# Kernel tuning notes

Measured on AMD Instinct MI355X. Metric: run time of the kernel, lower is better.

The kernel has to match this reference:

```python
import jax, jax.numpy as jnp
import numpy as np

N_NODES = 200000
N_EDGES = 6400000
N_GRAPHS = 512
VOCAB = 10
EMBED = 8
RLEN = 20
EPS = 1e-5


def setup_inputs() -> dict:
    key = jax.random.key(0)
    ks = jax.random.split(key, 16)
    f = lambda i, shape, s: jax.random.normal(ks[i], shape, jnp.float32) * s
    return {
        "x": jax.random.normal(ks[0], (N_NODES, 3), jnp.float32),
        "W1": f(1, (3, 64), 0.5), "b1": jnp.zeros((64,), jnp.float32),
        "gamma1": jnp.ones((64,), jnp.float32), "beta1": jnp.zeros((64,), jnp.float32),
        "W2": f(2, (64, 64), 0.12), "b2": jnp.zeros((64,), jnp.float32),
        "gamma2": jnp.ones((64,), jnp.float32), "beta2": jnp.zeros((64,), jnp.float32),
        "emb": f(3, (VOCAB, EMBED), 1.0),
        "conv_w": f(4, (16, EMBED, 3), 0.2), "conv_b": jnp.zeros((16,), jnp.float32),
        "fc_w": f(5, (16 * RLEN, 64), 0.06), "fc_b": jnp.zeros((64,), jnp.float32),
        "m1_w": f(6, (192, 128), 0.08), "m1_b": jnp.zeros((128,), jnp.float32),
        "m2_w": f(7, (128, 64), 0.1), "m2_b": jnp.zeros((64,), jnp.float32),
        "m3_w": f(8, (64, 3), 0.17), "m3_b": jnp.zeros((3,), jnp.float32),
        "edge_index": jax.random.randint(ks[9], (2, N_EDGES), 0, N_NODES),
        "batch": jnp.sort(jax.random.randint(ks[10], (N_NODES,), 0, N_GRAPHS)),
        "recipe": jax.random.randint(ks[11], (N_GRAPHS, RLEN), 0, VOCAB),
    }


def _gcn_aggregate(h, src, dst, dinv, n):
    # symmetric-normalized scatter-add: sum_j (d_i d_j)^{-1/2} h_j
    norm = dinv[src] * dinv[dst]
    return jax.ops.segment_sum(h[src] * norm[:, None], dst, num_segments=n)


def _bn(h, gamma, beta):
    mu = h.mean(0)
    var = h.var(0)  # biased variance, as torch BN uses for normalization
    return (h - mu) * jax.lax.rsqrt(var + EPS) * gamma + beta


def reference(x, W1, b1, gamma1, beta1, W2, b2, gamma2, beta2, emb,
              conv_w, conv_b, fc_w, fc_b, m1_w, m1_b, m2_w, m2_b, m3_w, m3_b,
              edge_index, batch, recipe):
    n = x.shape[0]
    loop = jnp.arange(n)
    src = jnp.concatenate([edge_index[0], loop])  # add self loops (GCNConv default)
    dst = jnp.concatenate([edge_index[1], loop])
    deg = jax.ops.segment_sum(jnp.ones_like(src, jnp.float32), dst, num_segments=n)
    dinv = jnp.where(deg > 0, jax.lax.rsqrt(deg), 0.0)

    h = _gcn_aggregate(x @ W1, src, dst, dinv, n) + b1
    h = jax.nn.relu(_bn(h, gamma1, beta1))
    h = _gcn_aggregate(h @ W2, src, dst, dinv, n) + b2
    h = jax.nn.relu(_bn(h, gamma2, beta2))

    counts = jax.ops.segment_sum(jnp.ones((n,), jnp.float32), batch, num_segments=N_GRAPHS)
    h_mean = jax.ops.segment_sum(h, batch, num_segments=N_GRAPHS) / jnp.maximum(counts, 1.0)[:, None]
    h_max = jax.ops.segment_max(h, batch, num_segments=N_GRAPHS)
    h_max = jnp.where(jnp.isfinite(h_max), h_max, 0.0)  # guard empty graphs
    h_graph = jnp.concatenate([h_mean, h_max], axis=1)  # [G, 128]

    r = emb[recipe].transpose(0, 2, 1)  # [G, embed, L]
    rc = jax.lax.conv_general_dilated(r, conv_w, window_strides=(1,), padding=[(1, 1)],
                                      dimension_numbers=("NCH", "OIH", "NCH"))
    rc = jax.nn.relu(rc + conv_b[None, :, None])  # [G, 16, L]
    r_flat = rc.reshape(rc.shape[0], -1)  # channel-major flatten, matches torch
    r_vec = jax.nn.relu(r_flat @ fc_w + fc_b)  # [G, 64]

    c = jnp.concatenate([h_graph, r_vec], axis=1)  # [G, 192]
    c = jax.nn.relu(c @ m1_w + m1_b)
    c = jax.nn.relu(c @ m2_w + m2_b)
    return c @ m3_w + m3_b  # [G, 3]
```

## Files before the change

kernel.cpp:

```cpp
#include <hip/hip_runtime.h>

#define N_NODES 200000
#define N_EDGES 6400000
#define N_GRAPHS 512
#define RLEN 20
#define EMBED 8
#define EPS 1e-5f

#define NPB 1024
#define NBKT ((N_NODES + NPB - 1) / NPB)
#define CHUNK 8192
#define CAP 36864

typedef unsigned short ushort_t;
typedef __attribute__((ext_vector_type(8))) short short8;
typedef __attribute__((ext_vector_type(4))) float f32x4;

__device__ inline ushort_t f32_to_bf16(float f) {
  unsigned u = __float_as_uint(f);
  unsigned r = (u + 0x7fff + ((u >> 16) & 1)) >> 16;
  return (ushort_t)r;
}
__device__ inline float bf16_to_f32(ushort_t us) {
  return __uint_as_float(((unsigned)us) << 16);
}
__device__ inline float bfu_lo(unsigned u) { return __uint_as_float(u << 16); }
__device__ inline float bfu_hi(unsigned u) { return __uint_as_float(u & 0xFFFF0000u); }


__global__ void __launch_bounds__(512) k_bscatter(const int* __restrict__ src,
                                                  const int* __restrict__ dst,
                                                  int* __restrict__ bcursor,
                                                  int* __restrict__ ebuf) {
  __shared__ int hist[8][256];
  __shared__ int gbase[256];
  int t = threadIdx.x;
  int wid = t >> 6;
  for (int i = t; i < 8 * 256; i += 512) ((int*)hist)[i] = 0;
  __syncthreads();

  const int4* src4 = (const int4*)(src + blockIdx.x * CHUNK);
  const int4* dst4 = (const int4*)(dst + blockIdx.x * CHUNK);
  int e0 = blockIdx.x * CHUNK;
  int nrem = N_EDGES - e0;
  int nv = (nrem >= CHUNK ? CHUNK : nrem) >> 2;

  int pk[16], bk[16], rk[16];
  #pragma unroll
  for (int g = 0; g < 4; ++g) {
    int vi = g * 512 + t;
    if (vi < nv) {
      int4 s4 = src4[vi];
      int4 d4 = dst4[vi];
      #pragma unroll
      for (int c = 0; c < 4; ++c) {
        int s = (&s4.x)[c], d = (&d4.x)[c];
        int b = d >> 10;
        pk[g * 4 + c] = s | ((d & (NPB - 1)) << 18);
        bk[g * 4 + c] = b;
        rk[g * 4 + c] = atomicAdd(&hist[wid][b], 1);
      }
    } else {
      #pragma unroll
      for (int c = 0; c < 4; ++c) bk[g * 4 + c] = -1;
    }
  }
  __syncthreads();
  if (t < 256) {
    int s = 0;
    #pragma unroll
    for (int w = 0; w < 8; ++w) { int v = hist[w][t]; hist[w][t] = s; s += v; }
    if (t < NBKT && s > 0) gbase[t] = t * CAP + atomicAdd(&bcursor[t], s);
  }
  __syncthreads();
  #pragma unroll
  for (int k = 0; k < 16; ++k) {
    if (bk[k] >= 0) ebuf[gbase[bk[k]] + hist[wid][bk[k]] + rk[k]] = pk[k];
  }
}

__global__ void __launch_bounds__(1024) k_bfill(const int* __restrict__ bcursor,
                                                const int* __restrict__ ebuf,
                                                const float* __restrict__ x,
                                                int* __restrict__ rowstart,
                                                int* __restrict__ rowlen,
                                                float* __restrict__ dinv,
                                                float4* __restrict__ xs,
                                                int* __restrict__ cols) {
  __shared__ int deg[NPB];
  __shared__ int cur[NPB];
  __shared__ int wsum[16];
  int b = blockIdx.x;
  int t = threadIdx.x;
  int lane = t & 63, wid = t >> 6;
  int estart = b * CAP;
  int cnt = bcursor[b];
  int eend = estart + cnt;
  int nv = cnt >> 2;
  const int4* eb4 = (const int4*)(ebuf + estart);
  deg[t] = 0;
  __syncthreads();
  for (int i = t; i < nv; i += 1024) {
    int4 p4 = eb4[i];
    atomicAdd(&deg[((unsigned)p4.x) >> 18], 1);
    atomicAdd(&deg[((unsigned)p4.y) >> 18], 1);
    atomicAdd(&deg[((unsigned)p4.z) >> 18], 1);
    atomicAdd(&deg[((unsigned)p4.w) >> 18], 1);
  }
  for (int i = estart + (nv << 2) + t; i < eend; i += 1024) {
    int p = ebuf[i];
    atomicAdd(&deg[((unsigned)p) >> 18], 1);
  }
  __syncthreads();
  int v = deg[t];
  int incl = v;
  #pragma unroll
  for (int off = 1; off < 64; off <<= 1) {
    int u = __shfl_up(incl, off);
    if (lane >= off) incl += u;
  }
  if (lane == 63) wsum[wid] = incl;
  __syncthreads();
  int wbase = 0;
  for (int w = 0; w < wid; ++w) wbase += wsum[w];
  int excl = wbase + incl - v;
  cur[t] = excl;
  int n = b * NPB + t;
  if (n < N_NODES) {
    rowstart[n] = estart + excl;
    rowlen[n] = v;
    float dv = rsqrtf((float)(v + 1));
    dinv[n] = dv;
    float4 o;
    o.x = x[n * 3 + 0] * dv;
    o.y = x[n * 3 + 1] * dv;
    o.z = x[n * 3 + 2] * dv;
    o.w = 0.f;
    xs[n] = o;
  }
  __syncthreads();
  for (int i = t; i < nv; i += 1024) {
    int4 p4 = eb4[i];
    #pragma unroll
    for (int c = 0; c < 4; ++c) {
      int p = (&p4.x)[c];
      int dl = ((unsigned)p) >> 18;
      int lpos = atomicAdd(&cur[dl], 1);
      cols[estart + lpos] = p & 0x3FFFF;
    }
  }
  for (int i = estart + (nv << 2) + t; i < eend; i += 1024) {
    int p = ebuf[i];
    int dl = ((unsigned)p) >> 18;
    int lpos = atomicAdd(&cur[dl], 1);
    cols[estart + lpos] = p & 0x3FFFF;
  }
}


__global__ void k_agg1(const float4* __restrict__ xs, float4* __restrict__ t,
                       const int* __restrict__ rowstart, const int* __restrict__ rowlen,
                       const int* __restrict__ cols,
                       const float* __restrict__ dinv, float* __restrict__ mom) {
  int n = blockIdx.x * blockDim.x + threadIdx.x;
  float m9[9] = {0.f, 0.f, 0.f, 0.f, 0.f, 0.f, 0.f, 0.f, 0.f};
  if (n < N_NODES) {
    float4 self = xs[n];
    float a0 = self.x, a1 = self.y, a2 = self.z;
    float b0 = 0.f, b1 = 0.f, b2 = 0.f;
    float c0 = 0.f, c1 = 0.f, c2 = 0.f;
    float e0 = 0.f, e1 = 0.f, e2 = 0.f;
    int base = rowstart[n];
    int len = rowlen[n];
    int j = 0;
    for (; j + 8 <= len; j += 8) {
      int s0 = cols[base + j],     s1 = cols[base + j + 1];
      int s2 = cols[base + j + 2], s3 = cols[base + j + 3];
      int s4 = cols[base + j + 4], s5 = cols[base + j + 5];
      int s6 = cols[base + j + 6], s7 = cols[base + j + 7];
      float4 v0 = xs[s0], v1 = xs[s1], v2 = xs[s2], v3 = xs[s3];
      float4 v4 = xs[s4], v5 = xs[s5], v6 = xs[s6], v7 = xs[s7];
      a0 += v0.x + v4.x; a1 += v0.y + v4.y; a2 += v0.z + v4.z;
      b0 += v1.x + v5.x; b1 += v1.y + v5.y; b2 += v1.z + v5.z;
      c0 += v2.x + v6.x; c1 += v2.y + v6.y; c2 += v2.z + v6.z;
      e0 += v3.x + v7.x; e1 += v3.y + v7.y; e2 += v3.z + v7.z;
    }
    for (; j + 4 <= len; j += 4) {
      int s0 = cols[base + j], s1 = cols[base + j + 1];
      int s2 = cols[base + j + 2], s3 = cols[base + j + 3];
      float4 v0 = xs[s0], v1 = xs[s1], v2 = xs[s2], v3 = xs[s3];
      a0 += v0.x; a1 += v0.y; a2 += v0.z;
      b0 += v1.x; b1 += v1.y; b2 += v1.z;
      c0 += v2.x; c1 += v2.y; c2 += v2.z;
      e0 += v3.x; e1 += v3.y; e2 += v3.z;
    }
    for (; j < len; ++j) {
      float4 v = xs[cols[base + j]];
      a0 += v.x; a1 += v.y; a2 += v.z;
    }
    float dv = dinv[n];
    float4 o;
    o.x = dv * ((a0 + b0) + (c0 + e0));
    o.y = dv * ((a1 + b1) + (c1 + e1));
    o.z = dv * ((a2 + b2) + (c2 + e2));
    o.w = 0.f;
    t[n] = o;
    m9[0] = o.x; m9[1] = o.y; m9[2] = o.z;
    m9[3] = o.x * o.x; m9[4] = o.x * o.y; m9[5] = o.x * o.z;
    m9[6] = o.y * o.y; m9[7] = o.y * o.z; m9[8] = o.z * o.z;
  }
  #pragma unroll
  for (int off = 32; off; off >>= 1) {
    #pragma unroll
    for (int i = 0; i < 9; ++i) m9[i] += __shfl_xor(m9[i], off);
  }
  __shared__ float ls[4][9];
  int lane = threadIdx.x & 63, wid = threadIdx.x >> 6;
  if (lane == 0) {
    #pragma unroll
    for (int i = 0; i < 9; ++i) ls[wid][i] = m9[i];
  }
  __syncthreads();
  if (threadIdx.x < 9) {
    float s = ls[0][threadIdx.x] + ls[1][threadIdx.x] + ls[2][threadIdx.x] + ls[3][threadIdx.x];
    atomicAdd(&mom[threadIdx.x], s);
  }
}

__global__ void __launch_bounds__(256) k_l2m2(const float4* __restrict__ t,
                                              ushort_t* __restrict__ hb,
                                              const float* __restrict__ W1,
                                              const float* __restrict__ W2,
                                              const float* __restrict__ mom,
                                              const float* __restrict__ gamma,
                                              const float* __restrict__ beta,
                                              const float* __restrict__ dinv) {
  __shared__ float w1s[192];
  __shared__ ushort_t w2t_hi[64 * 64];
  __shared__ ushort_t w2t_lo[64 * 64];
  __shared__ float tt[4][16][4];
  __shared__ ushort_t at_hi[4][16 * 64];
  __shared__ ushort_t at_lo[4][16 * 64];
  int tix = threadIdx.x;
  int lane = tix & 63, wid = tix >> 6;
  if (tix < 192) w1s[tix] = W1[tix];
  for (int i = tix; i < 64 * 64; i += 256) {
    int f = i >> 6, k = i & 63;
    float w = W2[k * 64 + f];
    ushort_t hi = f32_to_bf16(w);
    w2t_hi[i] = hi;
    w2t_lo[i] = f32_to_bf16(w - bf16_to_f32(hi));
  }
  __syncthreads();

  int col = lane & 15, kb = lane >> 4;
  short8 bhi[4][2], blo[4][2];
  #pragma unroll
  for (int nt = 0; nt < 4; ++nt) {
    #pragma unroll
    for (int ks = 0; ks < 2; ++ks) {
      int base = (nt * 16 + col) * 64 + ks * 32 + kb * 8;
      bhi[nt][ks] = *reinterpret_cast<const short8*>(&w2t_hi[base]);
      blo[nt][ks] = *reinterpret_cast<const short8*>(&w2t_lo[base]);
    }
  }

  float inv_n = 1.0f / N_NODES;
  float w0 = w1s[lane], w1 = w1s[64 + lane], w2 = w1s[128 + lane];
  float mu = (mom[0] * w0 + mom[1] * w1 + mom[2] * w2) * inv_n;
  float eh2 = (mom[3] * w0 * w0 + 2.f * mom[4] * w0 * w1 + 2.f * mom[5] * w0 * w2 +
               mom[6] * w1 * w1 + 2.f * mom[7] * w1 * w2 + mom[8] * w2 * w2) * inv_n;
  float var = eh2 - mu * mu;
  float sc = rsqrtf(var + EPS) * gamma[lane];
  float sh = beta[lane] - mu * sc;

  for (int bt = blockIdx.x; bt < 3125; bt += gridDim.x) {
    int n0 = (bt * 4 + wid) * 16;
    if (lane < 16) {
      float4 v = t[n0 + lane];
      tt[wid][lane][0] = v.x; tt[wid][lane][1] = v.y; tt[wid][lane][2] = v.z;
    }
    #pragma unroll 4
    for (int i = 0; i < 16; ++i) {
      float h = tt[wid][i][0] * w0 + tt[wid][i][1] * w1 + tt[wid][i][2] * w2;
      float a = h * sc + sh;
      a = a > 0.f ? a : 0.f;
      ushort_t hi = f32_to_bf16(a);
      at_hi[wid][i * 64 + lane] = hi;
      at_lo[wid][i * 64 + lane] = f32_to_bf16(a - bf16_to_f32(hi));
    }
    short8 ahi[2], alo[2];
    #pragma unroll
    for (int ks = 0; ks < 2; ++ks) {
      int base = col * 64 + ks * 32 + kb * 8;
      ahi[ks] = *reinterpret_cast<const short8*>(&at_hi[wid][base]);
      alo[ks] = *reinterpret_cast<const short8*>(&at_lo[wid][base]);
    }
    float dv[4];
    #pragma unroll
    for (int r = 0; r < 4; ++r) dv[r] = dinv[n0 + kb * 4 + r];

    #pragma unroll
    for (int nt = 0; nt < 4; ++nt) {
      f32x4 acc = {0.f, 0.f, 0.f, 0.f};
      #pragma unroll
      for (int ks = 0; ks < 2; ++ks) {
        acc = __builtin_amdgcn_mfma_f32_16x16x32_bf16(ahi[ks], bhi[nt][ks], acc, 0, 0, 0);
        acc = __builtin_amdgcn_mfma_f32_16x16x32_bf16(ahi[ks], blo[nt][ks], acc, 0, 0, 0);
        acc = __builtin_amdgcn_mfma_f32_16x16x32_bf16(alo[ks], bhi[nt][ks], acc, 0, 0, 0);
      }
      #pragma unroll
      for (int r = 0; r < 4; ++r) {
        int node = n0 + kb * 4 + r;
        int feat = nt * 16 + col;
        hb[node * 64 + feat] = f32_to_bf16(acc[r] * dv[r]);
      }
    }
  }
}

__global__ void k_agg2(const ushort_t* __restrict__ hb, ushort_t* __restrict__ h1b,
                       const int* __restrict__ rowstart, const int* __restrict__ rowlen,
                       const int* __restrict__ cols, const float* __restrict__ dinv) {
  int node = blockIdx.x * 4 + (threadIdx.x >> 6);
  int lane = threadIdx.x & 63;
  if (node >= N_NODES) return;
  int half = lane >> 5;
  int fl = lane & 31;
  const unsigned* hb32 = (const unsigned*)hb;
  unsigned* o32 = (unsigned*)h1b;
  float2 acc;
  if (half == 0) {
    unsigned u = hb32[node * 32 + fl];
    acc.x = bfu_lo(u); acc.y = bfu_hi(u);
  } else { acc.x = 0.f; acc.y = 0.f; }
  int base = rowstart[node];
  int len = rowlen[node];
  for (int c0 = 0; c0 < len; c0 += 64) {
    int rem = len - c0;
    int m = rem < 64 ? rem : 64;
    int cidx = (lane < m) ? cols[base + c0 + lane] : 0;
    int j = 0;
    for (; j + 8 <= m; j += 8) {
      int sA = __shfl(cidx, j + half);
      int sB = __shfl(cidx, j + 2 + half);
      int sC = __shfl(cidx, j + 4 + half);
      int sD = __shfl(cidx, j + 6 + half);
      unsigned uA = hb32[sA * 32 + fl], uB = hb32[sB * 32 + fl];
      unsigned uC = hb32[sC * 32 + fl], uD = hb32[sD * 32 + fl];
      acc.x += (bfu_lo(uA) + bfu_lo(uB)) + (bfu_lo(uC) + bfu_lo(uD));
      acc.y += (bfu_hi(uA) + bfu_hi(uB)) + (bfu_hi(uC) + bfu_hi(uD));
    }
    for (; j + 2 <= m; j += 2) {
      int s = __shfl(cidx, j + half);
      unsigned u = hb32[s * 32 + fl];
      acc.x += bfu_lo(u);
      acc.y += bfu_hi(u);
    }
    if (j < m) {
      int s = __shfl(cidx, j);
      if (half == 0) {
        unsigned u = hb32[s * 32 + fl];
        acc.x += bfu_lo(u);
        acc.y += bfu_hi(u);
      }
    }
  }
  acc.x += __shfl_xor(acc.x, 32);
  acc.y += __shfl_xor(acc.y, 32);
  if (half == 0) {
    float dv = dinv[node];
    float ox = acc.x * dv, oy = acc.y * dv;
    o32[node * 32 + fl] = ((unsigned)f32_to_bf16(oy) << 16) | (unsigned)f32_to_bf16(ox);
  }
}

__global__ void k_bnstats_b(const ushort_t* __restrict__ h1b, float* __restrict__ stats) {
  const unsigned* h32 = (const unsigned*)h1b;
  int tid = threadIdx.x;
  int lane = tid & 63, wid = tid >> 6;
  int fl = lane & 31, rsel = lane >> 5;
  float s0 = 0.f, s1 = 0.f, q0 = 0.f, q1 = 0.f;
  for (int r = blockIdx.x * 8 + wid * 2 + rsel; r < N_NODES; r += gridDim.x * 8) {
    unsigned u = h32[r * 32 + fl];
    float a = bfu_lo(u), b = bfu_hi(u);
    s0 += a; s1 += b; q0 += a * a; q1 += b * b;
  }
  s0 += __shfl_xor(s0, 32); s1 += __shfl_xor(s1, 32);
  q0 += __shfl_xor(q0, 32); q1 += __shfl_xor(q1, 32);
  __shared__ float ls[4][64], lq[4][64];
  if (rsel == 0) {
    ls[wid][2 * fl] = s0; ls[wid][2 * fl + 1] = s1;
    lq[wid][2 * fl] = q0; lq[wid][2 * fl + 1] = q1;
  }
  __syncthreads();
  if (tid < 64) {
    float a = ls[0][tid] + ls[1][tid] + ls[2][tid] + ls[3][tid];
    float b = lq[0][tid] + lq[1][tid] + lq[2][tid] + lq[3][tid];
    atomicAdd(&stats[tid], a);
    atomicAdd(&stats[64 + tid], b);
  }
}


__global__ void __launch_bounds__(256) k_poolhead(const ushort_t* __restrict__ h1b,
                                                  const float* __restrict__ stats2,
                                                  const float* __restrict__ gamma,
                                                  const float* __restrict__ beta,
                                                  const int* __restrict__ batch,
                                                  const int* __restrict__ recipe,
                                                  const float* __restrict__ emb,
                                                  const float* __restrict__ conv_w,
                                                  const float* __restrict__ conv_b,
                                                  const float* __restrict__ fc_w,
                                                  const float* __restrict__ fc_b,
                                                  const float* __restrict__ m1_w,
                                                  const float* __restrict__ m1_b,
                                                  const float* __restrict__ m2_w,
                                                  const float* __restrict__ m2_b,
                                                  const float* __restrict__ m3_w,
                                                  const float* __restrict__ m3_b,
                                                  float* __restrict__ out) {
  __shared__ float ssum[4][64], smax[4][64];
  __shared__ float cvec[192];
  __shared__ int sb[2];
  int g = blockIdx.x;
  int tid = threadIdx.x;
  int lane = tid & 63, wid = tid >> 6;

  if (tid < 2) {
    int tg = g + tid;
    int lo = 0, hi = N_NODES;
    while (lo < hi) {
      int mid = (lo + hi) >> 1;
      if (batch[mid] < tg) lo = mid + 1; else hi = mid;
    }
    sb[tid] = lo;
  }
  __syncthreads();
  int s0g = sb[0], s1g = sb[1];
  {
    float mu = stats2[lane] * (1.0f / N_NODES);
    float var = stats2[64 + lane] * (1.0f / N_NODES) - mu * mu;
    float sc = rsqrtf(var + EPS) * gamma[lane];
    float sh = beta[lane] - mu * sc;
    float sum = 0.f, mx = 0.f;
    for (int r = s0g + wid; r < s1g; r += 4) {
      float v = bf16_to_f32(h1b[r * 64 + lane]) * sc + sh;
      v = v > 0.f ? v : 0.f;
      sum += v;
      mx = v > mx ? v : mx;
    }
    ssum[wid][lane] = sum;
    smax[wid][lane] = mx;
  }
  __syncthreads();
  if (wid == 0) {
    float s = ssum[0][lane] + ssum[1][lane] + ssum[2][lane] + ssum[3][lane];
    float m = fmaxf(fmaxf(smax[0][lane], smax[1][lane]), fmaxf(smax[2][lane], smax[3][lane]));
    int cnt = s1g - s0g;
    float inv = 1.0f / (float)(cnt > 0 ? cnt : 1);
    cvec[lane] = s * inv;
    cvec[64 + lane] = m;
  }
  __syncthreads();

  __shared__ float r_s[RLEN][EMBED];
  __shared__ float convout[16 * RLEN];
  __shared__ float y1[128];
  __shared__ float y2[64];
  __shared__ int rec_s[RLEN];
  __shared__ float emb_s[80];
  if (tid < 80) emb_s[tid] = emb[tid];
  if (tid < RLEN) rec_s[tid] = recipe[g * RLEN + tid];
  __syncthreads();
  for (int idx = tid; idx < RLEN * EMBED; idx += blockDim.x) {
    int pos = idx >> 3, e = idx & 7;
    r_s[pos][e] = emb_s[rec_s[pos] * EMBED + e];
  }
  __syncthreads();
  for (int idx = tid; idx < 16 * RLEN; idx += blockDim.x) {
    int c = idx / RLEN, pos = idx % RLEN;
    float acc = conv_b[c];
    #pragma unroll
    for (int k = 0; k < 3; ++k) {
      int p = pos + k - 1;
      if (p >= 0 && p < RLEN) {
        #pragma unroll
        for (int e = 0; e < EMBED; ++e)
          acc = fmaf(r_s[p][e], conv_w[(c * EMBED + e) * 3 + k], acc);
      }
    }
    convout[c * RLEN + pos] = acc > 0.f ? acc : 0.f;
  }
  __syncthreads();
  if (tid < 64) {
    float acc = fc_b[tid];
    for (int i = 0; i < 320; ++i) acc = fmaf(convout[i], fc_w[i * 64 + tid], acc);
    cvec[128 + tid] = acc > 0.f ? acc : 0.f;
  }
  __syncthreads();
  if (tid < 128) {
    float acc = m1_b[tid];
    for (int i = 0; i < 192; ++i) acc = fmaf(cvec[i], m1_w[i * 128 + tid], acc);
    y1[tid] = acc > 0.f ? acc : 0.f;
  }
  __syncthreads();
  if (tid < 64) {
    float acc = m2_b[tid];
    for (int i = 0; i < 128; ++i) acc = fmaf(y1[i], m2_w[i * 64 + tid], acc);
    y2[tid] = acc > 0.f ? acc : 0.f;
  }
  __syncthreads();
  if (tid < 3) {
    float acc = m3_b[tid];
    for (int i = 0; i < 64; ++i) acc = fmaf(y2[i], m3_w[i * 3 + tid], acc);
    out[g * 3 + tid] = acc;
  }
}

extern "C" void kernel_launch(void* const* d_in, const int* in_sizes, int n_in,
                              void* d_out, int out_size, void* d_ws, size_t ws_size,
                              hipStream_t stream) {
  const float* x      = (const float*)d_in[0];
  const float* W1     = (const float*)d_in[1];
  const float* gamma1 = (const float*)d_in[3];
  const float* beta1  = (const float*)d_in[4];
  const float* W2     = (const float*)d_in[5];
  const float* gamma2 = (const float*)d_in[7];
  const float* beta2  = (const float*)d_in[8];
  const float* emb    = (const float*)d_in[9];
  const float* conv_w = (const float*)d_in[10];
  const float* conv_b = (const float*)d_in[11];
  const float* fc_w   = (const float*)d_in[12];
  const float* fc_b   = (const float*)d_in[13];
  const float* m1_w   = (const float*)d_in[14];
  const float* m1_b   = (const float*)d_in[15];
  const float* m2_w   = (const float*)d_in[16];
  const float* m2_b   = (const float*)d_in[17];
  const float* m3_w   = (const float*)d_in[18];
  const float* m3_b   = (const float*)d_in[19];
  const int* ei       = (const int*)d_in[20];
  const int* batch    = (const int*)d_in[21];
  const int* recipe   = (const int*)d_in[22];
  const int* e_src = ei;
  const int* e_dst = ei + N_EDGES;
  float* out = (float*)d_out;

  char* p = (char*)d_ws;
  auto alloc = [&](size_t bytes) {
    char* r = p;
    p += (bytes + 255) & ~(size_t)255;
    return (void*)r;
  };
  int*   bcursor  = (int*)alloc((size_t)NBKT * 4);
  float* stats    = (float*)alloc(256 * 4);
  float* mom      = (float*)alloc(16 * 4);
  float* dinv     = (float*)alloc((size_t)N_NODES * 4);
  int*   rowstart = (int*)alloc((size_t)N_NODES * 4);
  int*   rowlen   = (int*)alloc((size_t)N_NODES * 4);
  int*   cols     = (int*)alloc((size_t)NBKT * CAP * 4);
  float4* xs      = (float4*)alloc((size_t)N_NODES * 16);
  float4* tbuf    = (float4*)alloc((size_t)N_NODES * 16);
  int*   ebuf     = (int*)alloc((size_t)NBKT * CAP * 4);
  ushort_t* hb    = (ushort_t*)alloc((size_t)N_NODES * 64 * 2);
  ushort_t* h1b   = (ushort_t*)ebuf;

  hipMemsetAsync(bcursor, 0, 2304, stream);

  k_bscatter<<<(N_EDGES + CHUNK - 1) / CHUNK, 512, 0, stream>>>(e_src, e_dst, bcursor, ebuf);
  k_bfill<<<NBKT, 1024, 0, stream>>>(bcursor, ebuf, x, rowstart, rowlen, dinv, xs, cols);
  k_agg1<<<(N_NODES + 255) / 256, 256, 0, stream>>>(xs, tbuf, rowstart, rowlen, cols, dinv, mom);
  k_l2m2<<<625, 256, 0, stream>>>(tbuf, hb, W1, W2, mom, gamma1, beta1, dinv);
  k_agg2<<<(N_NODES + 3) / 4, 256, 0, stream>>>(hb, h1b, rowstart, rowlen, cols, dinv);
  k_bnstats_b<<<512, 256, 0, stream>>>(h1b, stats);
  k_poolhead<<<N_GRAPHS, 256, 0, stream>>>(h1b, stats, gamma2, beta2, batch, recipe, emb,
                                           conv_w, conv_b, fc_w, fc_b,
                                           m1_w, m1_b, m2_w, m2_b, m3_w, m3_b, out);
}
```

Baseline: 398.3 us.

## Aggregate layer-1 directly from destination buckets with shared-memory atomics

Replaces the CSR-based per-node gather for the first GCN aggregation with a per-bucket kernel. Each block reads the unsorted bucketed edge buffer and accumulates neighbour features into a shared-memory accumulator using LDS atomics, then writes normalized outputs and moment statistics. It avoids depending on the sorted column array for layer 1 and gives coalesced edge reads. The cost is heavy LDS atomic contention (three float atomics per edge) and float summation that is now non-deterministic. Because ebuf is still read here, h1b can no longer alias it and gets a separate allocation.

```diff
diff --git a/kernel.cpp b/kernel.cpp
--- a/kernel.cpp
+++ b/kernel.cpp
@@ -158,51 +158,55 @@
 }
 
 
-__global__ void k_agg1(const float4* __restrict__ xs, float4* __restrict__ t,
-                       const int* __restrict__ rowstart, const int* __restrict__ rowlen,
-                       const int* __restrict__ cols,
-                       const float* __restrict__ dinv, float* __restrict__ mom) {
-  int n = blockIdx.x * blockDim.x + threadIdx.x;
+__global__ void __launch_bounds__(1024) k_eagg1(const int* __restrict__ bcursor,
+                                                const int* __restrict__ ebuf,
+                                                const float4* __restrict__ xs,
+                                                const float* __restrict__ dinv,
+                                                float4* __restrict__ t,
+                                                float* __restrict__ mom) {
+  __shared__ float acc[NPB][4];
+  __shared__ float ls9[16][9];
+  int b = blockIdx.x;
+  int tid = threadIdx.x;
+  int lane = tid & 63, wid = tid >> 6;
+  int estart = b * CAP;
+  int cnt = bcursor[b];
+  int nv = cnt >> 2;
+  const int4* eb4 = (const int4*)(ebuf + estart);
+  acc[tid][0] = 0.f; acc[tid][1] = 0.f; acc[tid][2] = 0.f;
+  __syncthreads();
+  for (int i = tid; i < nv; i += 1024) {
+    int4 p4 = eb4[i];
+    #pragma unroll
+    for (int c = 0; c < 4; ++c) {
+      int p = (&p4.x)[c];
+      int s = p & 0x3FFFF;
+      int dl = ((unsigned)p) >> 18;
+      float4 v = xs[s];
+      atomicAdd(&acc[dl][0], v.x);
+      atomicAdd(&acc[dl][1], v.y);
+      atomicAdd(&acc[dl][2], v.z);
+    }
+  }
+  for (int i = estart + (nv << 2) + tid; i < estart + cnt; i += 1024) {
+    int p = ebuf[i];
+    int s = p & 0x3FFFF;
+    int dl = ((unsigned)p) >> 18;
+    float4 v = xs[s];
+    atomicAdd(&acc[dl][0], v.x);
+    atomicAdd(&acc[dl][1], v.y);
+    atomicAdd(&acc[dl][2], v.z);
+  }
+  __syncthreads();
   float m9[9] = {0.f, 0.f, 0.f, 0.f, 0.f, 0.f, 0.f, 0.f, 0.f};
+  int n = b * NPB + tid;
   if (n < N_NODES) {
     float4 self = xs[n];
-    float a0 = self.x, a1 = self.y, a2 = self.z;
-    float b0 = 0.f, b1 = 0.f, b2 = 0.f;
-    float c0 = 0.f, c1 = 0.f, c2 = 0.f;
-    float e0 = 0.f, e1 = 0.f, e2 = 0.f;
-    int base = rowstart[n];
-    int len = rowlen[n];
-    int j = 0;
-    for (; j + 8 <= len; j += 8) {
-      int s0 = cols[base + j],     s1 = cols[base + j + 1];
-      int s2 = cols[base + j + 2], s3 = cols[base + j + 3];
-      int s4 = cols[base + j + 4], s5 = cols[base + j + 5];
-      int s6 = cols[base + j + 6], s7 = cols[base + j + 7];
-      float4 v0 = xs[s0], v1 = xs[s1], v2 = xs[s2], v3 = xs[s3];
-      float4 v4 = xs[s4], v5 = xs[s5], v6 = xs[s6], v7 = xs[s7];
-      a0 += v0.x + v4.x; a1 += v0.y + v4.y; a2 += v0.z + v4.z;
-      b0 += v1.x + v5.x; b1 += v1.y + v5.y; b2 += v1.z + v5.z;
-      c0 += v2.x + v6.x; c1 += v2.y + v6.y; c2 += v2.z + v6.z;
-      e0 += v3.x + v7.x; e1 += v3.y + v7.y; e2 += v3.z + v7.z;
-    }
-    for (; j + 4 <= len; j += 4) {
-      int s0 = cols[base + j], s1 = cols[base + j + 1];
-      int s2 = cols[base + j + 2], s3 = cols[base + j + 3];
-      float4 v0 = xs[s0], v1 = xs[s1], v2 = xs[s2], v3 = xs[s3];
-      a0 += v0.x; a1 += v0.y; a2 += v0.z;
-      b0 += v1.x; b1 += v1.y; b2 += v1.z;
-      c0 += v2.x; c1 += v2.y; c2 += v2.z;
-      e0 += v3.x; e1 += v3.y; e2 += v3.z;
-    }
-    for (; j < len; ++j) {
-      float4 v = xs[cols[base + j]];
-      a0 += v.x; a1 += v.y; a2 += v.z;
-    }
     float dv = dinv[n];
     float4 o;
-    o.x = dv * ((a0 + b0) + (c0 + e0));
-    o.y = dv * ((a1 + b1) + (c1 + e1));
-    o.z = dv * ((a2 + b2) + (c2 + e2));
+    o.x = dv * (self.x + acc[tid][0]);
+    o.y = dv * (self.y + acc[tid][1]);
+    o.z = dv * (self.z + acc[tid][2]);
     o.w = 0.f;
     t[n] = o;
     m9[0] = o.x; m9[1] = o.y; m9[2] = o.z;
@@ -214,16 +218,16 @@
     #pragma unroll
     for (int i = 0; i < 9; ++i) m9[i] += __shfl_xor(m9[i], off);
   }
-  __shared__ float ls[4][9];
-  int lane = threadIdx.x & 63, wid = threadIdx.x >> 6;
   if (lane == 0) {
     #pragma unroll
-    for (int i = 0; i < 9; ++i) ls[wid][i] = m9[i];
-  }
-  __syncthreads();
-  if (threadIdx.x < 9) {
-    float s = ls[0][threadIdx.x] + ls[1][threadIdx.x] + ls[2][threadIdx.x] + ls[3][threadIdx.x];
-    atomicAdd(&mom[threadIdx.x], s);
+    for (int i = 0; i < 9; ++i) ls9[wid][i] = m9[i];
+  }
+  __syncthreads();
+  if (tid < 9) {
+    float s = 0.f;
+    #pragma unroll
+    for (int w = 0; w < 16; ++w) s += ls9[w][tid];
+    atomicAdd(&mom[tid], s);
   }
 }
 
@@ -564,13 +568,13 @@
   float4* tbuf    = (float4*)alloc((size_t)N_NODES * 16);
   int*   ebuf     = (int*)alloc((size_t)NBKT * CAP * 4);
   ushort_t* hb    = (ushort_t*)alloc((size_t)N_NODES * 64 * 2);
-  ushort_t* h1b   = (ushort_t*)ebuf;
+  ushort_t* h1b   = (ushort_t*)alloc((size_t)N_NODES * 64 * 2);
 
   hipMemsetAsync(bcursor, 0, 2304, stream);
 
   k_bscatter<<<(N_EDGES + CHUNK - 1) / CHUNK, 512, 0, stream>>>(e_src, e_dst, bcursor, ebuf);
   k_bfill<<<NBKT, 1024, 0, stream>>>(bcursor, ebuf, x, rowstart, rowlen, dinv, xs, cols);
-  k_agg1<<<(N_NODES + 255) / 256, 256, 0, stream>>>(xs, tbuf, rowstart, rowlen, cols, dinv, mom);
+  k_eagg1<<<NBKT, 1024, 0, stream>>>(bcursor, ebuf, xs, dinv, tbuf, mom);
   k_l2m2<<<625, 256, 0, stream>>>(tbuf, hb, W1, W2, mom, gamma1, beta1, dinv);
   k_agg2<<<(N_NODES + 3) / 4, 256, 0, stream>>>(hb, h1b, rowstart, rowlen, cols, dinv);
   k_bnstats_b<<<512, 256, 0, stream>>>(h1b, stats);
```

Result: slower. 472.5 us (+18.7%).
